# Kernel tuning notes

Measured on AMD Instinct MI355X. Metric: run time of the kernel, lower is better.

The kernel has to match this reference:

```python
import jax, jax.numpy as jnp
import numpy as np

N, L, C_IN, DEM = 64, 2048, 256, 10


def setup_inputs() -> dict:
    key = jax.random.key(0)
    k1, k2, k3, k4 = jax.random.split(key, 4)
    timesteps = jax.random.normal(k1, (N, L, C_IN), dtype=jnp.float32)
    dem = jax.random.normal(k2, (N, DEM), dtype=jnp.float32)
    W1 = jax.random.normal(k3, (DEM, 40), dtype=jnp.float32) * 0.1
    b1 = jnp.zeros((40,), dtype=jnp.float32)
    W2 = jax.random.normal(k4, (40, 20), dtype=jnp.float32) * 0.1
    b2 = jnp.zeros((20,), dtype=jnp.float32)
    return {"timesteps": timesteps, "dem": dem, "W1": W1, "b1": b1, "W2": W2, "b2": b2}


def reference(timesteps, dem, W1, b1, W2, b2):
    # dem MLP: Linear(10,40) -> ReLU -> (Dropout p=0, eval) -> Linear(40,20) -> ReLU
    h = jax.nn.relu(dem @ W1 + b1)
    dem_emb = jax.nn.relu(h @ W2 + b2)                     # (N, 20)
    n, l, _ = timesteps.shape
    dem_b = jnp.broadcast_to(dem_emb[:, None, :], (n, l, dem_emb.shape[-1]))
    x = jnp.concatenate([timesteps, dem_b], axis=-1)       # (N, L, C)
    # Causal nonzero-average pool: avg_pool1d with kernel=L over (L-1)-left-padded
    # sequence == at step t, sum(x[:t+1]) / count_nonzero(x[:t+1]) per channel.
    csum = jnp.cumsum(x, axis=1)                           # (N, L, C)
    ccnt = jnp.cumsum((x != 0).astype(x.dtype), axis=1)    # (N, L, C)
    p_avg = csum / jnp.maximum(ccnt, 1.0)
    return jax.nn.relu(p_avg)
```

## Files before the change

kernel.cpp:

```cpp
#include <hip/hip_runtime.h>


#define NB 64
#define LL 2048
#define CIN 256
#define COUT 276
#define DEMD 10
#define H1 40
#define H2 20

#define SEGS 64
#define SROWS (LL / SEGS)
#define UB 8
#define NBATCH (SROWS / UB)
#define NUNITS (NB * SEGS)
#define NBLK (NUNITS / 4)

typedef float vfloat4 __attribute__((ext_vector_type(4)));

static __device__ __forceinline__ void nt_store4(float* p, float4 v) {
    vfloat4 t = {v.x, v.y, v.z, v.w};
    __builtin_nontemporal_store(t, (vfloat4*)p);
}

__global__ __launch_bounds__(256) void pme_part(
    const float* __restrict__ ts,
    float* __restrict__ part)
{
    const int tid  = threadIdx.x;
    const int w    = tid >> 6;
    const int lane = tid & 63;

    const int unit = blockIdx.x * 4 + w;
    const int seg  = unit & (SEGS - 1);
    const int n    = unit >> 6;

    const float4* tp = (const float4*)(ts + ((size_t)n * LL + seg * SROWS) * CIN) + lane;

    float4 sum = make_float4(0.f, 0.f, 0.f, 0.f);
    float4 ctv = make_float4(0.f, 0.f, 0.f, 0.f);

    float4 v[2][UB];
#pragma unroll
    for (int u = 0; u < UB; ++u)
        v[0][u] = tp[(size_t)u * (CIN / 4)];

    for (int bb = 0; bb < NBATCH; ++bb) {
        const int cur = bb & 1;
        if (bb + 1 < NBATCH) {
#pragma unroll
            for (int u = 0; u < UB; ++u)
                v[cur ^ 1][u] = tp[(size_t)((bb + 1) * UB + u) * (CIN / 4)];
        }
#pragma unroll
        for (int u = 0; u < UB; ++u) {
            float4 x = v[cur][u];
            sum.x += x.x; ctv.x += (x.x != 0.f) ? 1.f : 0.f;
            sum.y += x.y; ctv.y += (x.y != 0.f) ? 1.f : 0.f;
            sum.z += x.z; ctv.z += (x.z != 0.f) ? 1.f : 0.f;
            sum.w += x.w; ctv.w += (x.w != 0.f) ? 1.f : 0.f;
        }
    }

    float4* pp = (float4*)part + ((size_t)n * SEGS + seg) * 128 + lane * 2;
    pp[0] = make_float4(sum.x, ctv.x, sum.y, ctv.y);
    pp[1] = make_float4(sum.z, ctv.z, sum.w, ctv.w);
}

__global__ __launch_bounds__(256) void pme_scan(
    const float* __restrict__ ts,
    const float* __restrict__ part,
    const float* __restrict__ dem,
    const float* __restrict__ W1, const float* __restrict__ b1,
    const float* __restrict__ W2, const float* __restrict__ b2,
    float* __restrict__ out)
{
    const int tid  = threadIdx.x;
    const int w    = tid >> 6;
    const int lane = tid & 63;

    const int unit = blockIdx.x * 4 + w;
    const int seg  = unit & (SEGS - 1);
    const int n    = unit >> 6;

    const float4* base = (const float4*)part + (size_t)n * SEGS * 128 + lane * 2;
    float4 A = make_float4(0.f, 0.f, 0.f, 0.f);
    float4 B = make_float4(0.f, 0.f, 0.f, 0.f);
    for (int s = 0; s < seg; ++s) {
        float4 a = base[(size_t)s * 128];
        float4 b = base[(size_t)s * 128 + 1];
        A.x += a.x; A.y += a.y; A.z += a.z; A.w += a.w;
        B.x += b.x; B.y += b.y; B.z += b.z; B.w += b.w;
    }
    float4 acc = make_float4(A.x, A.z, B.x, B.z);
    float4 cnt = make_float4(A.y, A.w, B.y, B.w);

    float4 e4q;
    {
        const float* dn = dem + n * DEMD;
        float d[DEMD];
#pragma unroll
        for (int i = 0; i < DEMD; ++i)
            d[i] = dn[i];
        const int q = (lane < 5) ? lane : 0;
        float e0 = b2[q * 4 + 0], e1 = b2[q * 4 + 1], e2 = b2[q * 4 + 2], e3 = b2[q * 4 + 3];
#pragma unroll
        for (int k = 0; k < H1; ++k) {
            float hk = b1[k];
#pragma unroll
            for (int i = 0; i < DEMD; ++i)
                hk += d[i] * W1[i * H1 + k];
            hk = fmaxf(hk, 0.f);
            e0 += hk * W2[k * H2 + q * 4 + 0];
            e1 += hk * W2[k * H2 + q * 4 + 1];
            e2 += hk * W2[k * H2 + q * 4 + 2];
            e3 += hk * W2[k * H2 + q * 4 + 3];
        }
        e4q = make_float4(fmaxf(e0, 0.f), fmaxf(e1, 0.f), fmaxf(e2, 0.f), fmaxf(e3, 0.f));
    }

    const float4* tp = (const float4*)(ts + ((size_t)n * LL + seg * SROWS) * CIN) + lane;
    float* oprow = out + ((size_t)n * LL + seg * SROWS) * COUT;

    float4 v[2][UB];
#pragma unroll
    for (int u = 0; u < UB; ++u)
        v[0][u] = tp[(size_t)u * (CIN / 4)];

    for (int bb = 0; bb < NBATCH; ++bb) {
        const int cur = bb & 1;
        if (bb + 1 < NBATCH) {
#pragma unroll
            for (int u = 0; u < UB; ++u)
                v[cur ^ 1][u] = tp[(size_t)((bb + 1) * UB + u) * (CIN / 4)];
        }
#pragma unroll
        for (int u = 0; u < UB; ++u) {
            float4 x = v[cur][u];
            float4 r;
            acc.x += x.x; cnt.x += (x.x != 0.f) ? 1.f : 0.f;
            acc.y += x.y; cnt.y += (x.y != 0.f) ? 1.f : 0.f;
            acc.z += x.z; cnt.z += (x.z != 0.f) ? 1.f : 0.f;
            acc.w += x.w; cnt.w += (x.w != 0.f) ? 1.f : 0.f;
            r.x = fmaxf(acc.x * __builtin_amdgcn_rcpf(fmaxf(cnt.x, 1.f)), 0.f);
            r.y = fmaxf(acc.y * __builtin_amdgcn_rcpf(fmaxf(cnt.y, 1.f)), 0.f);
            r.z = fmaxf(acc.z * __builtin_amdgcn_rcpf(fmaxf(cnt.z, 1.f)), 0.f);
            r.w = fmaxf(acc.w * __builtin_amdgcn_rcpf(fmaxf(cnt.w, 1.f)), 0.f);
            float* rowp = oprow + (size_t)(bb * UB + u) * COUT;
            nt_store4(rowp + lane * 4, r);
            if (lane < 5)
                nt_store4(rowp + CIN + lane * 4, e4q);
        }
    }
}

extern "C" void kernel_launch(void* const* d_in, const int* in_sizes, int n_in,
                              void* d_out, int out_size, void* d_ws, size_t ws_size,
                              hipStream_t stream) {
    const float* ts  = (const float*)d_in[0];
    const float* dem = (const float*)d_in[1];
    const float* W1  = (const float*)d_in[2];
    const float* b1  = (const float*)d_in[3];
    const float* W2  = (const float*)d_in[4];
    const float* b2  = (const float*)d_in[5];
    float* out  = (float*)d_out;
    float* part = (float*)d_ws;

    pme_part<<<NBLK, 256, 0, stream>>>(ts, part);
    pme_scan<<<NBLK, 256, 0, stream>>>(ts, part, dem, W1, b1, W2, b2, out);
}
```

Before: 286.6 us.

## Parallelize prefix scan across waves and batch dem-embedding tail stores

The serial cross-segment prefix loop, which ran up to 63 iterations in late segments, is split so that each of the 4 waves sums a quarter of the preceding group range. The partial sums are combined through shared memory, and only the in-group remainder is added serially. The 20-column dem-embedding tail is no longer written by 5 lanes on every row; it is written once after the main loop, with 60 lanes covering 12 rows per store. Nontemporal stores are also replaced by ordinary stores, which changes cache behaviour on the large output stream.

Measured after the change: 300.6 us. 1.05x slower.

```diff
diff --git a/kernel.cpp b/kernel.cpp
--- a/kernel.cpp
+++ b/kernel.cpp
@@ -15,13 +15,6 @@
 #define NBATCH (SROWS / UB)
 #define NUNITS (NB * SEGS)
 #define NBLK (NUNITS / 4)
-
-typedef float vfloat4 __attribute__((ext_vector_type(4)));
-
-static __device__ __forceinline__ void nt_store4(float* p, float4 v) {
-    vfloat4 t = {v.x, v.y, v.z, v.w};
-    __builtin_nontemporal_store(t, (vfloat4*)p);
-}
 
 __global__ __launch_bounds__(256) void pme_part(
     const float* __restrict__ ts,
@@ -75,26 +68,54 @@
     const float* __restrict__ W2, const float* __restrict__ b2,
     float* __restrict__ out)
 {
+    __shared__ float4 QS[4][64];
+    __shared__ float4 QC[4][64];
+
     const int tid  = threadIdx.x;
     const int w    = tid >> 6;
     const int lane = tid & 63;
 
-    const int unit = blockIdx.x * 4 + w;
-    const int seg  = unit & (SEGS - 1);
-    const int n    = unit >> 6;
+    const int b       = blockIdx.x;
+    const int n       = b >> 4;
+    const int grp     = b & 15;
+    const int segbase = grp * 4;
+    const int seg     = segbase + w;
+    const int q       = grp;
 
     const float4* base = (const float4*)part + (size_t)n * SEGS * 128 + lane * 2;
+
     float4 A = make_float4(0.f, 0.f, 0.f, 0.f);
     float4 B = make_float4(0.f, 0.f, 0.f, 0.f);
-    for (int s = 0; s < seg; ++s) {
+    for (int s = w * q; s < w * q + q; ++s) {
         float4 a = base[(size_t)s * 128];
-        float4 b = base[(size_t)s * 128 + 1];
+        float4 c = base[(size_t)s * 128 + 1];
         A.x += a.x; A.y += a.y; A.z += a.z; A.w += a.w;
-        B.x += b.x; B.y += b.y; B.z += b.z; B.w += b.w;
+        B.x += c.x; B.y += c.y; B.z += c.z; B.w += c.w;
+    }
+    QS[w][lane] = A;
+    QC[w][lane] = B;
+    __syncthreads();
+
+    A = make_float4(0.f, 0.f, 0.f, 0.f);
+    B = make_float4(0.f, 0.f, 0.f, 0.f);
+#pragma unroll
+    for (int s = 0; s < 4; ++s) {
+        float4 a = QS[s][lane];
+        float4 c = QC[s][lane];
+        A.x += a.x; A.y += a.y; A.z += a.z; A.w += a.w;
+        B.x += c.x; B.y += c.y; B.z += c.z; B.w += c.w;
+    }
+    for (int s = segbase; s < seg; ++s) {
+        float4 a = base[(size_t)s * 128];
+        float4 c = base[(size_t)s * 128 + 1];
+        A.x += a.x; A.y += a.y; A.z += a.z; A.w += a.w;
+        B.x += c.x; B.y += c.y; B.z += c.z; B.w += c.w;
     }
     float4 acc = make_float4(A.x, A.z, B.x, B.z);
     float4 cnt = make_float4(A.y, A.w, B.y, B.w);
 
+    const int tr = lane / 5;
+    const int tj = lane - tr * 5;
     float4 e4q;
     {
         const float* dn = dem + n * DEMD;
@@ -102,8 +123,7 @@
 #pragma unroll
         for (int i = 0; i < DEMD; ++i)
             d[i] = dn[i];
-        const int q = (lane < 5) ? lane : 0;
-        float e0 = b2[q * 4 + 0], e1 = b2[q * 4 + 1], e2 = b2[q * 4 + 2], e3 = b2[q * 4 + 3];
+        float e0 = b2[tj * 4 + 0], e1 = b2[tj * 4 + 1], e2 = b2[tj * 4 + 2], e3 = b2[tj * 4 + 3];
 #pragma unroll
         for (int k = 0; k < H1; ++k) {
             float hk = b1[k];
@@ -111,10 +131,10 @@
             for (int i = 0; i < DEMD; ++i)
                 hk += d[i] * W1[i * H1 + k];
             hk = fmaxf(hk, 0.f);
-            e0 += hk * W2[k * H2 + q * 4 + 0];
-            e1 += hk * W2[k * H2 + q * 4 + 1];
-            e2 += hk * W2[k * H2 + q * 4 + 2];
-            e3 += hk * W2[k * H2 + q * 4 + 3];
+            e0 += hk * W2[k * H2 + tj * 4 + 0];
+            e1 += hk * W2[k * H2 + tj * 4 + 1];
+            e2 += hk * W2[k * H2 + tj * 4 + 2];
+            e3 += hk * W2[k * H2 + tj * 4 + 3];
         }
         e4q = make_float4(fmaxf(e0, 0.f), fmaxf(e1, 0.f), fmaxf(e2, 0.f), fmaxf(e3, 0.f));
     }
@@ -146,12 +166,17 @@
             r.y = fmaxf(acc.y * __builtin_amdgcn_rcpf(fmaxf(cnt.y, 1.f)), 0.f);
             r.z = fmaxf(acc.z * __builtin_amdgcn_rcpf(fmaxf(cnt.z, 1.f)), 0.f);
             r.w = fmaxf(acc.w * __builtin_amdgcn_rcpf(fmaxf(cnt.w, 1.f)), 0.f);
-            float* rowp = oprow + (size_t)(bb * UB + u) * COUT;
-            nt_store4(rowp + lane * 4, r);
-            if (lane < 5)
-                nt_store4(rowp + CIN + lane * 4, e4q);
+            *(float4*)(oprow + (size_t)(bb * UB + u) * COUT + lane * 4) = r;
         }
     }
+
+    float* tailbase = oprow + CIN;
+    if (lane < 60) {
+        *(float4*)(tailbase + (size_t)(0  + tr) * COUT + tj * 4) = e4q;
+        *(float4*)(tailbase + (size_t)(12 + tr) * COUT + tj * 4) = e4q;
+    }
+    if (lane < 40)
+        *(float4*)(tailbase + (size_t)(24 + tr) * COUT + tj * 4) = e4q;
 }
 
 extern "C" void kernel_launch(void* const* d_in, const int* in_sizes, int n_in,
```
